# Performance work log

Hardware: AMD Instinct MI355X
Metric: run time of the kernel (lower is better)

Reference implementation:

```python
import jax, jax.numpy as jnp
import numpy as np

HIDDEN = 1024
N_HEADS = 16
HEAD_DIM = HIDDEN // N_HEADS
SCALE = HEAD_DIM ** (-0.5)


def setup_inputs() -> dict:
    key = jax.random.key(0)
    k1, k2, k3 = jax.random.split(key, 3)
    x = jax.random.normal(k1, (2, 2048, HIDDEN), dtype=jnp.float32)
    w_qkv = jax.random.normal(k2, (HIDDEN, 3 * HIDDEN), dtype=jnp.float32) * (HIDDEN ** -0.5)
    b_qkv = jnp.zeros((3 * HIDDEN,), dtype=jnp.float32)
    w_proj = jax.random.normal(k3, (HIDDEN, HIDDEN), dtype=jnp.float32) * (HIDDEN ** -0.5)
    b_proj = jnp.zeros((HIDDEN,), dtype=jnp.float32)
    return {"x": x, "w_qkv": w_qkv, "b_qkv": b_qkv, "w_proj": w_proj, "b_proj": b_proj}


def reference(x, w_qkv, b_qkv, w_proj, b_proj):
    b, n, dim = x.shape
    qkv = x @ w_qkv + b_qkv                              # (b, n, 3*dim)
    qkv = qkv.reshape(b, n, 3, N_HEADS, HEAD_DIM)
    qkv = jnp.transpose(qkv, (2, 0, 3, 1, 4))            # (3, b, h, n, d)
    q, k, v = qkv[0], qkv[1], qkv[2]
    dp = jnp.einsum('bhqd,bhkd->bhqk', q, k) * SCALE     # (b, h, n, n)
    # NOTE: original applies softmax over dim=1 == the HEADS axis (non-standard)
    attn = jax.nn.softmax(dp, axis=1)
    w_avg = jnp.einsum('bhqk,bhkd->bhqd', attn, v)       # (b, h, n, d)
    w_avg = jnp.transpose(w_avg, (0, 2, 1, 3)).reshape(b, n, dim)
    out = w_avg @ w_proj + b_proj
    return out
```

## Files before the change

### kernel.cpp

```cpp
#include <hip/hip_runtime.h>

typedef unsigned short u16;
typedef unsigned int u32;
typedef __attribute__((ext_vector_type(8))) short bf16x8;
typedef __attribute__((ext_vector_type(4))) float f32x4;
typedef __attribute__((ext_vector_type(8))) u16 u16x8;
typedef __attribute__((ext_vector_type(2))) u32 u32x2;

__device__ __forceinline__ u16 f2b(float f){
  u32 u = __float_as_uint(f);
  u32 r = (u + 0x7fffu + ((u >> 16) & 1u)) >> 16;
  return (u16)r;
}
__device__ __forceinline__ float b2f(u16 h){ return __uint_as_float(((u32)h) << 16); }
__device__ __forceinline__ u32 cvt_pk_bf16(float lo, float hi){
  u32 r; asm("v_cvt_pk_bf16_f32 %0, %1, %2" : "=v"(r) : "v"(lo), "v"(hi)); return r;
}
__device__ __forceinline__ void lds_barrier(){
  asm volatile("s_waitcnt lgkmcnt(0)" ::: "memory");
  __builtin_amdgcn_s_barrier();
  asm volatile("" ::: "memory");
}

typedef const __attribute__((address_space(1))) void gvoid;
typedef __attribute__((address_space(3))) void svoid;
__device__ __forceinline__ void gl_lds16(const void* g, void* l){
  __builtin_amdgcn_global_load_lds((gvoid*)g, (svoid*)l, 16, 0, 0);
}

__global__ void conv_f2b(const float* __restrict__ in, u16* __restrict__ out, int n8){
  int i = blockIdx.x * 256 + threadIdx.x;
  if(i >= n8) return;
  f32x4 a = *(const f32x4*)(in + (size_t)i*8);
  f32x4 b = *(const f32x4*)(in + (size_t)i*8 + 4);
  u16x8 o;
  #pragma unroll
  for(int j=0;j<4;j++){ o[j] = f2b(a[j]); o[4+j] = f2b(b[j]); }
  *(u16x8*)(out + (size_t)i*8) = o;
}

__global__ void tconv(const float* __restrict__ in, u16* __restrict__ out, int R, int C){
  __shared__ __align__(16) float tile[64*68];
  int gc = C >> 6;
  int rt = blockIdx.x / gc, ct = blockIdx.x % gc;
  int r0 = rt*64, c0 = ct*64;
  int tid = threadIdx.x;
  #pragma unroll
  for(int it=0; it<4; it++){
    int idx = tid + it*256;
    int rl = idx >> 4, cseg = idx & 15;
    f32x4 v = *(const f32x4*)(in + (size_t)(r0+rl)*C + c0 + cseg*4);
    *(f32x4*)&tile[rl*68 + cseg*4] = v;
  }
  __syncthreads();
  #pragma unroll
  for(int it=0; it<2; it++){
    int idx = tid + it*256;
    int cl = idx >> 3, rseg = idx & 7;
    u16x8 o;
    #pragma unroll
    for(int j=0;j<8;j++) o[j] = f2b(tile[(rseg*8+j)*68 + cl]);
    *(u16x8*)(out + (size_t)(c0+cl)*R + r0 + rseg*8) = o;
  }
}

template<int EPI>
__global__ __launch_bounds__(256,2) void gemm_bt(const u16* __restrict__ A, const u16* __restrict__ Bt,
                                                 void* __restrict__ Cp, const float* __restrict__ bias,
                                                 int M, int N, int K){
  __shared__ __align__(16) u16 As[128*32];
  __shared__ __align__(16) u16 Bs[128*32];
  int tid = threadIdx.x, lane = tid & 63, w = tid >> 6;
  int nb = N >> 7;
  int bm = blockIdx.x / nb, bn = blockIdx.x % nb;
  int m0 = bm*128, n0 = bn*128;
  int wm = (w >> 1)*64, wn = (w & 1)*64;
  int l16 = lane & 15, lg = lane >> 4;
  f32x4 acc[4][4];
  #pragma unroll
  for(int i=0;i<4;i++)
    #pragma unroll
    for(int j=0;j<4;j++) acc[i][j] = (f32x4){0.f,0.f,0.f,0.f};

  for(int kk=0; kk<K; kk+=32){
    #pragma unroll
    for(int it=0; it<2; it++){
      int id = tid + it*256;
      int row = id >> 2, seg = id & 3;
      gl_lds16(A  + (size_t)(m0+row)*K + kk + seg*8, &As[id*8]);
      gl_lds16(Bt + (size_t)(n0+row)*K + kk + seg*8, &Bs[id*8]);
    }
    __syncthreads();
    bf16x8 af[4], bfr[4];
    #pragma unroll
    for(int i=0;i<4;i++) af[i]  = *(const bf16x8*)&As[(wm + i*16 + l16)*32 + lg*8];
    #pragma unroll
    for(int j=0;j<4;j++) bfr[j] = *(const bf16x8*)&Bs[(wn + j*16 + l16)*32 + lg*8];
    #pragma unroll
    for(int i=0;i<4;i++)
      #pragma unroll
      for(int j=0;j<4;j++)
        acc[i][j] = __builtin_amdgcn_mfma_f32_16x16x32_bf16(af[i], bfr[j], acc[i][j], 0,0,0);
    __syncthreads();
  }
  #pragma unroll
  for(int i=0;i<4;i++)
    #pragma unroll
    for(int j=0;j<4;j++){
      int col = n0 + wn + j*16 + l16;
      #pragma unroll
      for(int r=0;r<4;r++){
        int row = m0 + wm + i*16 + lg*4 + r;
        float v = acc[i][j][r];
        if(EPI == 0) ((u16*)Cp)[(size_t)row*N + col] = f2b(v);
        else         ((float*)Cp)[(size_t)row*N + col] = v + bias[col];
      }
    }
}

__global__ __launch_bounds__(256,2) void gemm_qkv(const u16* __restrict__ A, const u16* __restrict__ Bt,
                                                  const float* __restrict__ bias,
                                                  u16* __restrict__ Qs, u16* __restrict__ Ks,
                                                  u16* __restrict__ Vout){
  const int N = 3072, K = 1024;
  __shared__ __align__(16) u16 As[128*32];
  __shared__ __align__(16) u16 Bs[128*32];
  int tid = threadIdx.x, lane = tid & 63, w = tid >> 6;
  int nb = N >> 7;
  int bm = blockIdx.x / nb, bn = blockIdx.x % nb;
  int m0 = bm*128, n0 = bn*128;
  int wm = (w >> 1)*64, wn = (w & 1)*64;
  int l16 = lane & 15, lg = lane >> 4;
  f32x4 acc[4][4];
  #pragma unroll
  for(int i=0;i<4;i++)
    #pragma unroll
    for(int j=0;j<4;j++) acc[i][j] = (f32x4){0.f,0.f,0.f,0.f};

  for(int kk=0; kk<K; kk+=32){
    #pragma unroll
    for(int it=0; it<2; it++){
      int id = tid + it*256;
      int row = id >> 2, seg = id & 3;
      gl_lds16(A  + (size_t)(m0+row)*K + kk + seg*8, &As[id*8]);
      gl_lds16(Bt + (size_t)(n0+row)*K + kk + seg*8, &Bs[id*8]);
    }
    __syncthreads();
    bf16x8 af[4], bfr[4];
    #pragma unroll
    for(int i=0;i<4;i++) af[i]  = *(const bf16x8*)&As[(wm + i*16 + l16)*32 + lg*8];
    #pragma unroll
    for(int j=0;j<4;j++) bfr[j] = *(const bf16x8*)&Bs[(wn + j*16 + l16)*32 + lg*8];
    #pragma unroll
    for(int i=0;i<4;i++)
      #pragma unroll
      for(int j=0;j<4;j++)
        acc[i][j] = __builtin_amdgcn_mfma_f32_16x16x32_bf16(af[i], bfr[j], acc[i][j], 0,0,0);
    __syncthreads();
  }
  #pragma unroll
  for(int i=0;i<4;i++)
    #pragma unroll
    for(int j=0;j<4;j++){
      int col = n0 + wn + j*16 + l16;
      int which = col >> 10;
      int hd = col & 1023;
      int h = hd >> 6, d = hd & 63;
      float bcol = bias[col];
      float scale = (which == 0) ? 0.18033688011112042f : 1.0f;
      #pragma unroll
      for(int r=0;r<4;r++){
        int row = m0 + wm + i*16 + lg*4 + r;
        float v = (acc[i][j][r] + bcol) * scale;
        if(which == 2){
          Vout[(size_t)row*3072 + col] = f2b(v);
        } else {
          int b = row >> 11, n = row & 2047;
          u16* dst = (which ? Ks : Qs);
          dst[((size_t)(b*16 + h)*2048 + n)*64 + d] = f2b(v);
        }
      }
    }
}

__global__ void transpose_v(const u16* __restrict__ qkv, u16* __restrict__ Vt){
  __shared__ __align__(16) u16 tile[64*72];
  int nt = blockIdx.x & 31, bh = blockIdx.x >> 5;
  int b = bh >> 4, h = bh & 15;
  int n0 = nt*64;
  int tid = threadIdx.x;
  const u16* src = qkv + (size_t)(b*2048)*3072 + 2048 + h*64;
  #pragma unroll
  for(int it=0; it<2; it++){
    int idx = tid + it*256;
    int nl = idx >> 3, dseg = idx & 7;
    u16x8 vv = *(const u16x8*)(src + (size_t)(n0+nl)*3072 + dseg*8);
    *(u16x8*)&tile[nl*72 + dseg*8] = vv;
  }
  __syncthreads();
  u16* dst = Vt + (size_t)bh*64*2048;
  #pragma unroll
  for(int it=0; it<2; it++){
    int idx = tid + it*256;
    int dl = idx >> 3, nseg = idx & 7;
    u16x8 o;
    #pragma unroll
    for(int j=0;j<8;j++) o[j] = tile[(nseg*8+j)*72 + dl];
    *(u16x8*)(dst + (size_t)dl*2048 + n0 + nseg*8) = o;
  }
}

__global__ __launch_bounds__(512,2) void attn_kernel(const u16* __restrict__ Q, const u16* __restrict__ Kg,
                                                     const u16* __restrict__ Vt, u16* __restrict__ Op){
  __shared__ float zsum[8*1024];
  __shared__ float rz[1024];
  const int tid = threadIdx.x, lane = tid & 63, w = tid >> 6;
  const int l16 = lane & 15, lg = lane >> 4;
  const int bid = blockIdx.x;
  const int split = bid & 1, qt = (bid >> 1) & 63, b = bid >> 7;
  const int q0 = qt*32;
  const int kbase = split*1024;

  const u16* Kh[2]; const u16* Vh[2];
  #pragma unroll
  for(int hh=0;hh<2;hh++){
    int h = w*2 + hh;
    Kh[hh] = Kg + (size_t)(b*16 + h)*2048*64;
    Vh[hh] = Vt + (size_t)(b*16 + h)*64*2048;
  }

  bf16x8 qf[2][2][2];
  #pragma unroll
  for(int hh=0;hh<2;hh++){
    int h = w*2 + hh;
    const u16* Qh = Q + ((size_t)(b*16 + h)*2048 + q0)*64;
    #pragma unroll
    for(int qs=0;qs<2;qs++)
      #pragma unroll
      for(int dc=0;dc<2;dc++)
        qf[hh][qs][dc] = *(const bf16x8*)(Qh + (qs*16 + l16)*64 + dc*32 + lg*8);
  }
  f32x4 Oa[2][4][2];
  #pragma unroll
  for(int a=0;a<2;a++)
    #pragma unroll
    for(int d=0;d<4;d++)
      #pragma unroll
      for(int c=0;c<2;c++) Oa[a][d][c] = (f32x4){0.f,0.f,0.f,0.f};

  bf16x8 kfb[2][2][2][2];
  #pragma unroll
  for(int hh=0;hh<2;hh++)
    #pragma unroll
    for(int ks=0;ks<2;ks++)
      #pragma unroll
      for(int dc=0;dc<2;dc++)
        kfb[0][hh][ks][dc] = *(const bf16x8*)(Kh[hh] + (size_t)(kbase + ks*16 + l16)*64 + dc*32 + lg*8);

  const int bp0 = ((2*(lg & 1))*16 + l16)*4;
  const int bp1 = bp0 + 64;

  #pragma unroll 2
  for(int kt=0; kt<32; kt++){
    const int cur = kt & 1, nxt = cur ^ 1;
    const int k0 = kbase + kt*32;
    const int k1 = (kt == 31) ? kbase : k0 + 32;

    bf16x8 vf[2][4];
    #pragma unroll
    for(int hh=0;hh<2;hh++)
      #pragma unroll
      for(int dt=0;dt<4;dt++)
        vf[hh][dt] = *(const bf16x8*)(Vh[hh] + (size_t)(dt*16 + l16)*2048 + k0 + lg*8);

    float p[2][2][2][4];
    #pragma unroll
    for(int hh=0;hh<2;hh++)
      #pragma unroll
      for(int qs=0;qs<2;qs++)
        #pragma unroll
        for(int ks=0;ks<2;ks++){
          f32x4 S = (f32x4){0.f,0.f,0.f,0.f};
          #pragma unroll
          for(int dc=0;dc<2;dc++)
            S = __builtin_amdgcn_mfma_f32_16x16x32_bf16(kfb[cur][hh][ks][dc], qf[hh][qs][dc], S, 0,0,0);
          #pragma unroll
          for(int r=0;r<4;r++) p[hh][qs][ks][r] = __builtin_amdgcn_exp2f(S[r]);
        }

    #pragma unroll
    for(int qs=0;qs<2;qs++)
      #pragma unroll
      for(int ks=0;ks<2;ks++)
        #pragma unroll
        for(int r=0;r<4;r++)
          zsum[w*1024 + (qs*2+ks)*256 + r*64 + lane] = p[0][qs][ks][r] + p[1][qs][ks][r];

    #pragma unroll
    for(int hh=0;hh<2;hh++)
      #pragma unroll
      for(int ks=0;ks<2;ks++)
        #pragma unroll
        for(int dc=0;dc<2;dc++)
          kfb[nxt][hh][ks][dc] = *(const bf16x8*)(Kh[hh] + (size_t)(k1 + ks*16 + l16)*64 + dc*32 + lg*8);

    lds_barrier();
    #pragma unroll
    for(int rr=0; rr<2; rr++){
      int s = tid + rr*512;
      float z = 0.f;
      #pragma unroll
      for(int wv=0; wv<8; wv++) z += zsum[wv*1024 + s];
      rz[s] = __builtin_amdgcn_rcpf(z);
    }
    lds_barrier();

    #pragma unroll
    for(int hh=0;hh<2;hh++){
      #pragma unroll
      for(int qs=0;qs<2;qs++){
        u32 Wa[2], Wb[2];
        #pragma unroll
        for(int ks=0;ks<2;ks++){
          float pn[4];
          #pragma unroll
          for(int r=0;r<4;r++)
            pn[r] = p[hh][qs][ks][r] * rz[(qs*2+ks)*256 + r*64 + lane];
          Wa[ks] = cvt_pk_bf16(pn[0], pn[1]);
          Wb[ks] = cvt_pk_bf16(pn[2], pn[3]);
        }
        bool lo = (lg < 2);
        u32 t0a = __builtin_amdgcn_ds_bpermute(bp0, (int)Wa[0]);
        u32 t0b = __builtin_amdgcn_ds_bpermute(bp0, (int)Wa[1]);
        u32 t1a = __builtin_amdgcn_ds_bpermute(bp0, (int)Wb[0]);
        u32 t1b = __builtin_amdgcn_ds_bpermute(bp0, (int)Wb[1]);
        u32 t2a = __builtin_amdgcn_ds_bpermute(bp1, (int)Wa[0]);
        u32 t2b = __builtin_amdgcn_ds_bpermute(bp1, (int)Wa[1]);
        u32 t3a = __builtin_amdgcn_ds_bpermute(bp1, (int)Wb[0]);
        u32 t3b = __builtin_amdgcn_ds_bpermute(bp1, (int)Wb[1]);
        union { u32 wd[4]; bf16x8 v; } U;
        U.wd[0] = lo ? t0a : t0b;
        U.wd[1] = lo ? t1a : t1b;
        U.wd[2] = lo ? t2a : t2b;
        U.wd[3] = lo ? t3a : t3b;
        #pragma unroll
        for(int dt=0;dt<4;dt++)
          Oa[hh][dt][qs] = __builtin_amdgcn_mfma_f32_16x16x32_bf16(vf[hh][dt], U.v, Oa[hh][dt][qs], 0,0,0);
      }
    }
  }
  u16* Ob = Op + (size_t)split*4194304;
  #pragma unroll
  for(int hh=0;hh<2;hh++){
    int h = w*2 + hh;
    #pragma unroll
    for(int dt=0;dt<4;dt++)
      #pragma unroll
      for(int qs=0;qs<2;qs++){
        int row = q0 + qs*16 + l16;
        int col = h*64 + dt*16 + lg*4;
        u32x2 pk2;
        pk2[0] = cvt_pk_bf16(Oa[hh][dt][qs][0], Oa[hh][dt][qs][1]);
        pk2[1] = cvt_pk_bf16(Oa[hh][dt][qs][2], Oa[hh][dt][qs][3]);
        *(u32x2*)(Ob + (size_t)(b*2048 + row)*1024 + col) = pk2;
      }
  }
}

__global__ void combine2(const u16* __restrict__ a, const u16* __restrict__ b, u16* __restrict__ o){
  int i = blockIdx.x * 256 + threadIdx.x;
  u16x8 va = ((const u16x8*)a)[i], vb = ((const u16x8*)b)[i];
  u16x8 vo;
  #pragma unroll
  for(int j=0;j<8;j++) vo[j] = f2b(b2f(va[j]) + b2f(vb[j]));
  ((u16x8*)o)[i] = vo;
}

extern "C" void kernel_launch(void* const* d_in, const int* in_sizes, int n_in,
                              void* d_out, int out_size, void* d_ws, size_t ws_size,
                              hipStream_t stream){
  const float* x      = (const float*)d_in[0];
  const float* w_qkv  = (const float*)d_in[1];
  const float* b_qkv  = (const float*)d_in[2];
  const float* w_proj = (const float*)d_in[3];
  const float* b_proj = (const float*)d_in[4];
  float* out = (float*)d_out;
  char* ws = (char*)d_ws;

  u16* xb   = (u16*)(ws);
  u16* wqT  = (u16*)(ws + 8388608);
  u16* wpT  = (u16*)(ws + 14680064);
  u16* Qs   = (u16*)(ws + 16777216);
  u16* Ks   = (u16*)(ws + 25165824);
  u16* Vt   = (u16*)(ws + 33554432);
  u16* qkvb = (u16*)(ws + 41943040);
  u16* Op0  = qkvb;
  u16* Op1  = qkvb + 4194304;
  u16* wavg = xb;

  conv_f2b<<<2048, 256, 0, stream>>>(x, xb, 524288);
  tconv<<<768, 256, 0, stream>>>(w_qkv, wqT, 1024, 3072);
  tconv<<<256, 256, 0, stream>>>(w_proj, wpT, 1024, 1024);
  gemm_qkv<<<768, 256, 0, stream>>>(xb, wqT, b_qkv, Qs, Ks, qkvb);
  transpose_v<<<1024, 256, 0, stream>>>(qkvb, Vt);
  attn_kernel<<<256, 512, 0, stream>>>(Qs, Ks, Vt, Op0);
  combine2<<<2048, 256, 0, stream>>>(Op0, Op1, wavg);
  gemm_bt<1><<<256, 256, 0, stream>>>(wavg, wpT, (void*)out, b_proj, 4096, 1024, 1024);
}
```

Baseline: 215.6 us.

## Assign one head per wave with 1024-thread attention blocks

The attention kernel now launches 1024 threads per block, with each of the 16 waves handling a single head instead of two heads per wave across 8 waves. The per-wave exp values are written to LDS as packed bf16 pairs, which halves the shared-memory footprint of the head-axis softmax sum, and 512 threads reduce over 16 waves. K-fragment double buffering and the unroll-by-2 are dropped. The aim is more wave-level parallelism and fewer registers per wave, at the cost of larger barriers, lower-precision partial sums, and less latency hiding.

```diff
diff --git a/kernel.cpp b/kernel.cpp
--- a/kernel.cpp
+++ b/kernel.cpp
@@ -210,9 +210,9 @@
   }
 }
 
-__global__ __launch_bounds__(512,2) void attn_kernel(const u16* __restrict__ Q, const u16* __restrict__ Kg,
-                                                     const u16* __restrict__ Vt, u16* __restrict__ Op){
-  __shared__ float zsum[8*1024];
+__global__ __launch_bounds__(1024) void attn_kernel(const u16* __restrict__ Q, const u16* __restrict__ Kg,
+                                                    const u16* __restrict__ Vt, u16* __restrict__ Op){
+  __shared__ u32 zsum32[16*512];
   __shared__ float rz[1024];
   const int tid = threadIdx.x, lane = tid & 63, w = tid >> 6;
   const int l16 = lane & 15, lg = lane >> 4;
@@ -220,151 +220,133 @@
   const int split = bid & 1, qt = (bid >> 1) & 63, b = bid >> 7;
   const int q0 = qt*32;
   const int kbase = split*1024;
-
-  const u16* Kh[2]; const u16* Vh[2];
-  #pragma unroll
-  for(int hh=0;hh<2;hh++){
-    int h = w*2 + hh;
-    Kh[hh] = Kg + (size_t)(b*16 + h)*2048*64;
-    Vh[hh] = Vt + (size_t)(b*16 + h)*64*2048;
-  }
-
-  bf16x8 qf[2][2][2];
-  #pragma unroll
-  for(int hh=0;hh<2;hh++){
-    int h = w*2 + hh;
+  const int h = w;
+
+  const u16* Kh = Kg + (size_t)(b*16 + h)*2048*64;
+  const u16* Vh = Vt + (size_t)(b*16 + h)*64*2048;
+
+  bf16x8 qf[2][2];
+  {
     const u16* Qh = Q + ((size_t)(b*16 + h)*2048 + q0)*64;
     #pragma unroll
     for(int qs=0;qs<2;qs++)
       #pragma unroll
       for(int dc=0;dc<2;dc++)
-        qf[hh][qs][dc] = *(const bf16x8*)(Qh + (qs*16 + l16)*64 + dc*32 + lg*8);
-  }
-  f32x4 Oa[2][4][2];
-  #pragma unroll
-  for(int a=0;a<2;a++)
-    #pragma unroll
-    for(int d=0;d<4;d++)
-      #pragma unroll
-      for(int c=0;c<2;c++) Oa[a][d][c] = (f32x4){0.f,0.f,0.f,0.f};
-
-  bf16x8 kfb[2][2][2][2];
-  #pragma unroll
-  for(int hh=0;hh<2;hh++)
-    #pragma unroll
-    for(int ks=0;ks<2;ks++)
-      #pragma unroll
-      for(int dc=0;dc<2;dc++)
-        kfb[0][hh][ks][dc] = *(const bf16x8*)(Kh[hh] + (size_t)(kbase + ks*16 + l16)*64 + dc*32 + lg*8);
+        qf[qs][dc] = *(const bf16x8*)(Qh + (qs*16 + l16)*64 + dc*32 + lg*8);
+  }
+  f32x4 Oa[4][2];
+  #pragma unroll
+  for(int d=0;d<4;d++)
+    #pragma unroll
+    for(int c=0;c<2;c++) Oa[d][c] = (f32x4){0.f,0.f,0.f,0.f};
+
+  bf16x8 kf[2][2];
+  #pragma unroll
+  for(int ks=0;ks<2;ks++)
+    #pragma unroll
+    for(int dc=0;dc<2;dc++)
+      kf[ks][dc] = *(const bf16x8*)(Kh + (size_t)(kbase + ks*16 + l16)*64 + dc*32 + lg*8);
 
   const int bp0 = ((2*(lg & 1))*16 + l16)*4;
   const int bp1 = bp0 + 64;
 
-  #pragma unroll 2
   for(int kt=0; kt<32; kt++){
-    const int cur = kt & 1, nxt = cur ^ 1;
     const int k0 = kbase + kt*32;
     const int k1 = (kt == 31) ? kbase : k0 + 32;
 
-    bf16x8 vf[2][4];
-    #pragma unroll
-    for(int hh=0;hh<2;hh++)
-      #pragma unroll
-      for(int dt=0;dt<4;dt++)
-        vf[hh][dt] = *(const bf16x8*)(Vh[hh] + (size_t)(dt*16 + l16)*2048 + k0 + lg*8);
-
-    float p[2][2][2][4];
-    #pragma unroll
-    for(int hh=0;hh<2;hh++)
-      #pragma unroll
-      for(int qs=0;qs<2;qs++)
+    bf16x8 vf[4];
+    #pragma unroll
+    for(int dt=0;dt<4;dt++)
+      vf[dt] = *(const bf16x8*)(Vh + (size_t)(dt*16 + l16)*2048 + k0 + lg*8);
+
+    float p[2][2][4];
+    #pragma unroll
+    for(int qs=0;qs<2;qs++)
+      #pragma unroll
+      for(int ks=0;ks<2;ks++){
+        f32x4 S = (f32x4){0.f,0.f,0.f,0.f};
         #pragma unroll
-        for(int ks=0;ks<2;ks++){
-          f32x4 S = (f32x4){0.f,0.f,0.f,0.f};
-          #pragma unroll
-          for(int dc=0;dc<2;dc++)
-            S = __builtin_amdgcn_mfma_f32_16x16x32_bf16(kfb[cur][hh][ks][dc], qf[hh][qs][dc], S, 0,0,0);
-          #pragma unroll
-          for(int r=0;r<4;r++) p[hh][qs][ks][r] = __builtin_amdgcn_exp2f(S[r]);
-        }
+        for(int dc=0;dc<2;dc++)
+          S = __builtin_amdgcn_mfma_f32_16x16x32_bf16(kf[ks][dc], qf[qs][dc], S, 0,0,0);
+        #pragma unroll
+        for(int r=0;r<4;r++) p[qs][ks][r] = __builtin_amdgcn_exp2f(S[r]);
+      }
+
+    #pragma unroll
+    for(int ks=0;ks<2;ks++)
+      #pragma unroll
+      for(int dc=0;dc<2;dc++)
+        kf[ks][dc] = *(const bf16x8*)(Kh + (size_t)(k1 + ks*16 + l16)*64 + dc*32 + lg*8);
 
     #pragma unroll
     for(int qs=0;qs<2;qs++)
       #pragma unroll
       for(int ks=0;ks<2;ks++)
         #pragma unroll
+        for(int rr=0;rr<2;rr++)
+          zsum32[w*512 + (qs*2+ks)*128 + rr*64 + lane] =
+            cvt_pk_bf16(p[qs][ks][2*rr], p[qs][ks][2*rr+1]);
+
+    lds_barrier();
+    if(tid < 512){
+      float zlo = 0.f, zhi = 0.f;
+      #pragma unroll
+      for(int wv=0; wv<16; wv++){
+        u32 v = zsum32[wv*512 + tid];
+        zlo += b2f((u16)v);
+        zhi += b2f((u16)(v >> 16));
+      }
+      int g = tid >> 7, rem = tid & 127;
+      int rr = rem >> 6, ln = rem & 63;
+      int base = g*256 + rr*128 + ln;
+      rz[base]      = __builtin_amdgcn_rcpf(zlo);
+      rz[base + 64] = __builtin_amdgcn_rcpf(zhi);
+    }
+    lds_barrier();
+
+    #pragma unroll
+    for(int qs=0;qs<2;qs++){
+      u32 Wa[2], Wb[2];
+      #pragma unroll
+      for(int ks=0;ks<2;ks++){
+        float pn[4];
+        #pragma unroll
         for(int r=0;r<4;r++)
-          zsum[w*1024 + (qs*2+ks)*256 + r*64 + lane] = p[0][qs][ks][r] + p[1][qs][ks][r];
-
-    #pragma unroll
-    for(int hh=0;hh<2;hh++)
-      #pragma unroll
-      for(int ks=0;ks<2;ks++)
-        #pragma unroll
-        for(int dc=0;dc<2;dc++)
-          kfb[nxt][hh][ks][dc] = *(const bf16x8*)(Kh[hh] + (size_t)(k1 + ks*16 + l16)*64 + dc*32 + lg*8);
-
-    lds_barrier();
-    #pragma unroll
-    for(int rr=0; rr<2; rr++){
-      int s = tid + rr*512;
-      float z = 0.f;
-      #pragma unroll
-      for(int wv=0; wv<8; wv++) z += zsum[wv*1024 + s];
-      rz[s] = __builtin_amdgcn_rcpf(z);
-    }
-    lds_barrier();
-
-    #pragma unroll
-    for(int hh=0;hh<2;hh++){
-      #pragma unroll
-      for(int qs=0;qs<2;qs++){
-        u32 Wa[2], Wb[2];
-        #pragma unroll
-        for(int ks=0;ks<2;ks++){
-          float pn[4];
-          #pragma unroll
-          for(int r=0;r<4;r++)
-            pn[r] = p[hh][qs][ks][r] * rz[(qs*2+ks)*256 + r*64 + lane];
-          Wa[ks] = cvt_pk_bf16(pn[0], pn[1]);
-          Wb[ks] = cvt_pk_bf16(pn[2], pn[3]);
-        }
-        bool lo = (lg < 2);
-        u32 t0a = __builtin_amdgcn_ds_bpermute(bp0, (int)Wa[0]);
-        u32 t0b = __builtin_amdgcn_ds_bpermute(bp0, (int)Wa[1]);
-        u32 t1a = __builtin_amdgcn_ds_bpermute(bp0, (int)Wb[0]);
-        u32 t1b = __builtin_amdgcn_ds_bpermute(bp0, (int)Wb[1]);
-        u32 t2a = __builtin_amdgcn_ds_bpermute(bp1, (int)Wa[0]);
-        u32 t2b = __builtin_amdgcn_ds_bpermute(bp1, (int)Wa[1]);
-        u32 t3a = __builtin_amdgcn_ds_bpermute(bp1, (int)Wb[0]);
-        u32 t3b = __builtin_amdgcn_ds_bpermute(bp1, (int)Wb[1]);
-        union { u32 wd[4]; bf16x8 v; } U;
-        U.wd[0] = lo ? t0a : t0b;
-        U.wd[1] = lo ? t1a : t1b;
-        U.wd[2] = lo ? t2a : t2b;
-        U.wd[3] = lo ? t3a : t3b;
-        #pragma unroll
-        for(int dt=0;dt<4;dt++)
-          Oa[hh][dt][qs] = __builtin_amdgcn_mfma_f32_16x16x32_bf16(vf[hh][dt], U.v, Oa[hh][dt][qs], 0,0,0);
-      }
+          pn[r] = p[qs][ks][r] * rz[(qs*2+ks)*256 + r*64 + lane];
+        Wa[ks] = cvt_pk_bf16(pn[0], pn[1]);
+        Wb[ks] = cvt_pk_bf16(pn[2], pn[3]);
+      }
+      bool lo = (lg < 2);
+      u32 t0a = __builtin_amdgcn_ds_bpermute(bp0, (int)Wa[0]);
+      u32 t0b = __builtin_amdgcn_ds_bpermute(bp0, (int)Wa[1]);
+      u32 t1a = __builtin_amdgcn_ds_bpermute(bp0, (int)Wb[0]);
+      u32 t1b = __builtin_amdgcn_ds_bpermute(bp0, (int)Wb[1]);
+      u32 t2a = __builtin_amdgcn_ds_bpermute(bp1, (int)Wa[0]);
+      u32 t2b = __builtin_amdgcn_ds_bpermute(bp1, (int)Wa[1]);
+      u32 t3a = __builtin_amdgcn_ds_bpermute(bp1, (int)Wb[0]);
+      u32 t3b = __builtin_amdgcn_ds_bpermute(bp1, (int)Wb[1]);
+      union { u32 wd[4]; bf16x8 v; } U;
+      U.wd[0] = lo ? t0a : t0b;
+      U.wd[1] = lo ? t1a : t1b;
+      U.wd[2] = lo ? t2a : t2b;
+      U.wd[3] = lo ? t3a : t3b;
+      #pragma unroll
+      for(int dt=0;dt<4;dt++)
+        Oa[dt][qs] = __builtin_amdgcn_mfma_f32_16x16x32_bf16(vf[dt], U.v, Oa[dt][qs], 0,0,0);
     }
   }
   u16* Ob = Op + (size_t)split*4194304;
   #pragma unroll
-  for(int hh=0;hh<2;hh++){
-    int h = w*2 + hh;
-    #pragma unroll
-    for(int dt=0;dt<4;dt++)
-      #pragma unroll
-      for(int qs=0;qs<2;qs++){
-        int row = q0 + qs*16 + l16;
-        int col = h*64 + dt*16 + lg*4;
-        u32x2 pk2;
-        pk2[0] = cvt_pk_bf16(Oa[hh][dt][qs][0], Oa[hh][dt][qs][1]);
-        pk2[1] = cvt_pk_bf16(Oa[hh][dt][qs][2], Oa[hh][dt][qs][3]);
-        *(u32x2*)(Ob + (size_t)(b*2048 + row)*1024 + col) = pk2;
-      }
-  }
+  for(int dt=0;dt<4;dt++)
+    #pragma unroll
+    for(int qs=0;qs<2;qs++){
+      int row = q0 + qs*16 + l16;
+      int col = h*64 + dt*16 + lg*4;
+      u32x2 pk2;
+      pk2[0] = cvt_pk_bf16(Oa[dt][qs][0], Oa[dt][qs][1]);
+      pk2[1] = cvt_pk_bf16(Oa[dt][qs][2], Oa[dt][qs][3]);
+      *(u32x2*)(Ob + (size_t)(b*2048 + row)*1024 + col) = pk2;
+    }
 }
 
 __global__ void combine2(const u16* __restrict__ a, const u16* __restrict__ b, u16* __restrict__ o){
@@ -403,7 +385,7 @@
   tconv<<<256, 256, 0, stream>>>(w_proj, wpT, 1024, 1024);
   gemm_qkv<<<768, 256, 0, stream>>>(xb, wqT, b_qkv, Qs, Ks, qkvb);
   transpose_v<<<1024, 256, 0, stream>>>(qkvb, Vt);
-  attn_kernel<<<256, 512, 0, stream>>>(Qs, Ks, Vt, Op0);
+  attn_kernel<<<256, 1024, 0, stream>>>(Qs, Ks, Vt, Op0);
   combine2<<<2048, 256, 0, stream>>>(Op0, Op1, wavg);
   gemm_bt<1><<<256, 256, 0, stream>>>(wavg, wpT, (void*)out, b_proj, 4096, 1024, 1024);
 }
```

Result: no change. 217.1 us (+0.7%).
